# Performance work log

Measured on AMD Instinct MI355X. Metric: run time of the kernel, lower is better.

## Reference

```python
import jax, jax.numpy as jnp
import numpy as np

N = 2_000_000  # total nodes across batch
F = 16         # eigenvector coefficient dim
B = 8          # number of graphs in batch (2^B sign combos)

def setup_inputs() -> dict:
    key = jax.random.key(0)
    k1, k2, k3 = jax.random.split(key, 3)
    inp = jax.random.normal(k1, (N, F), dtype=jnp.float32)
    tgt = jax.random.normal(k2, (N, F), dtype=jnp.float32)
    batch = jnp.sort(jax.random.randint(k3, (N,), 0, B, dtype=jnp.int32))
    return {"input": inp, "target": tgt, "batch": batch, "batch_size": B}

def reference(input, target, batch, batch_size):
    # loss(s) = sum((s_{batch} * x - t)^2) = sum(x^2) + sum(t^2) - 2 * sum_g s_g * dot_g
    # where dot_g = sum_{i in graph g} <x_i, t_i>.  Min over s in {+1,-1}^B is the
    # exact value produced by the original 2^B brute-force loop (reduction='sum').
    per_node = jnp.sum(input * target, axis=-1)                      # [N]
    dots = jax.ops.segment_sum(per_node, batch, num_segments=batch_size)  # [B]
    base = jnp.sum(input * input) + jnp.sum(target * target)         # scalar
    # enumerate all 2^B sign combinations (tiny, graph-level)
    idx = jnp.arange(2 ** batch_size)
    bits = (idx[:, None] >> jnp.arange(batch_size)[None, :]) & 1     # [2^B, B]
    signs = (1 - 2 * bits).astype(dots.dtype)                        # {+1,-1}
    losses = base - 2.0 * (signs @ dots)                             # [2^B]
    return jnp.min(losses)
```

## Files before the change

### kernel.cpp

```cpp
#include <hip/hip_runtime.h>

#define BLOCK 256
#define GRID  2048
#define NGRAPH 8


__global__ __launch_bounds__(BLOCK) void reduce_kernel(
    const float4* __restrict__ x4,
    const float4* __restrict__ t4,
    const int*    __restrict__ batch,
    float* __restrict__ g_acc,
    long long M )
{
    __shared__ float s_dots[NGRAPH];
    __shared__ float s_base;
    const int tid = threadIdx.x;
    if (tid < NGRAPH) s_dots[tid] = 0.0f;
    if (tid == 0)     s_base = 0.0f;
    __syncthreads();

    const long long stride = (long long)gridDim.x * (long long)blockDim.x;
    const long long start  = (long long)blockIdx.x * blockDim.x + tid;
    const long long M_pad = ((M + stride - 1) / stride) * stride;

    float base = 0.0f;

    for (long long e = start; e < M_pad; e += stride) {
        const bool valid = (e < M);
        float4 a = make_float4(0.f, 0.f, 0.f, 0.f);
        float4 c = make_float4(0.f, 0.f, 0.f, 0.f);
        int b = 0;
        if (valid) {
            a = x4[e];
            c = t4[e];
            b = batch[e >> 2];
        }
        base += a.x*a.x + a.y*a.y + a.z*a.z + a.w*a.w
              + c.x*c.x + c.y*c.y + c.z*c.z + c.w*c.w;
        float d = a.x*c.x + a.y*c.y + a.z*c.z + a.w*c.w;

        const int b0 = __builtin_amdgcn_readfirstlane(b);
        if (__all(b == b0)) {
            for (int off = 32; off > 0; off >>= 1)
                d += __shfl_xor(d, off, 64);
            if ((tid & 63) == 0)
                atomicAdd(&s_dots[b0], d);
        } else {
            atomicAdd(&s_dots[b], d);
        }
    }

    for (int off = 32; off > 0; off >>= 1)
        base += __shfl_xor(base, off, 64);
    if ((tid & 63) == 0)
        atomicAdd(&s_base, base);
    __syncthreads();

    if (tid < NGRAPH) atomicAdd(&g_acc[tid], s_dots[tid]);
    if (tid == 0)     atomicAdd(&g_acc[NGRAPH], s_base);
}

__global__ void finalize_kernel(const float* __restrict__ g_acc,
                                float* __restrict__ out)
{
    if (threadIdx.x == 0) {
        float s = 0.0f;
        #pragma unroll
        for (int i = 0; i < NGRAPH; ++i) s += fabsf(g_acc[i]);
        out[0] = g_acc[NGRAPH] - 2.0f * s;
    }
}

extern "C" void kernel_launch(void* const* d_in, const int* in_sizes, int n_in,
                              void* d_out, int out_size, void* d_ws, size_t ws_size,
                              hipStream_t stream) {
    const float* inp   = (const float*)d_in[0];
    const float* tgt   = (const float*)d_in[1];
    const int*   batch = (const int*)d_in[2];

    const long long Nrows = (long long)in_sizes[0] / 16;
    const long long M     = Nrows * 4;

    float* g_acc = (float*)d_ws;
    hipMemsetAsync(g_acc, 0, (NGRAPH + 1) * sizeof(float), stream);

    reduce_kernel<<<GRID, BLOCK, 0, stream>>>(
        (const float4*)inp, (const float4*)tgt, batch, g_acc, M);

    finalize_kernel<<<1, 64, 0, stream>>>(g_acc, (float*)d_out);
}
```

Measured before the change: 305.0 us.

## Use per-thread graph accumulators and fuse finalize via last-block counter

Replaces the per-iteration wave-uniform check, shuffle reduction and shared atomics with eight per-thread register accumulators selected by predication, and reduces them once at the end. The finalize kernel is folded into the reduce kernel through a global arrival counter, so the last block computes the output. This removes per-element shuffle and atomic overhead and one kernel launch, at the cost of more registers and some extra predicated adds per element.

Result: slower. 554.5 us (+81.8%).

```diff
diff --git a/kernel.cpp b/kernel.cpp
--- a/kernel.cpp
+++ b/kernel.cpp
@@ -10,64 +10,61 @@
     const float4* __restrict__ t4,
     const int*    __restrict__ batch,
     float* __restrict__ g_acc,
+    float* __restrict__ out,
     long long M )
 {
-    __shared__ float s_dots[NGRAPH];
-    __shared__ float s_base;
+    __shared__ float s_acc[NGRAPH + 1];
     const int tid = threadIdx.x;
-    if (tid < NGRAPH) s_dots[tid] = 0.0f;
-    if (tid == 0)     s_base = 0.0f;
+    if (tid < NGRAPH + 1) s_acc[tid] = 0.0f;
     __syncthreads();
 
-    const long long stride = (long long)gridDim.x * (long long)blockDim.x;
-    const long long start  = (long long)blockIdx.x * blockDim.x + tid;
-    const long long M_pad = ((M + stride - 1) / stride) * stride;
-
+    float acc[NGRAPH];
+    #pragma unroll
+    for (int i = 0; i < NGRAPH; ++i) acc[i] = 0.0f;
     float base = 0.0f;
 
-    for (long long e = start; e < M_pad; e += stride) {
-        const bool valid = (e < M);
-        float4 a = make_float4(0.f, 0.f, 0.f, 0.f);
-        float4 c = make_float4(0.f, 0.f, 0.f, 0.f);
-        int b = 0;
-        if (valid) {
-            a = x4[e];
-            c = t4[e];
-            b = batch[e >> 2];
-        }
+    const long long stride = (long long)gridDim.x * (long long)blockDim.x;
+    for (long long e = (long long)blockIdx.x * blockDim.x + tid; e < M; e += stride) {
+        const float4 a = x4[e];
+        const float4 c = t4[e];
+        const int   b  = batch[e >> 2];
+
         base += a.x*a.x + a.y*a.y + a.z*a.z + a.w*a.w
               + c.x*c.x + c.y*c.y + c.z*c.z + c.w*c.w;
-        float d = a.x*c.x + a.y*c.y + a.z*c.z + a.w*c.w;
+        const float d = a.x*c.x + a.y*c.y + a.z*c.z + a.w*c.w;
 
-        const int b0 = __builtin_amdgcn_readfirstlane(b);
-        if (__all(b == b0)) {
-            for (int off = 32; off > 0; off >>= 1)
-                d += __shfl_xor(d, off, 64);
-            if ((tid & 63) == 0)
-                atomicAdd(&s_dots[b0], d);
-        } else {
-            atomicAdd(&s_dots[b], d);
-        }
+        #pragma unroll
+        for (int i = 0; i < NGRAPH; ++i)
+            acc[i] += (b == i) ? d : 0.0f;
     }
 
-    for (int off = 32; off > 0; off >>= 1)
-        base += __shfl_xor(base, off, 64);
-    if ((tid & 63) == 0)
-        atomicAdd(&s_base, base);
+    #pragma unroll
+    for (int i = 0; i <= NGRAPH; ++i) {
+        float v = (i < NGRAPH) ? acc[i] : base;
+        #pragma unroll
+        for (int off = 32; off > 0; off >>= 1)
+            v += __shfl_xor(v, off, 64);
+        if ((tid & 63) == 0)
+            atomicAdd(&s_acc[i], v);
+    }
     __syncthreads();
 
-    if (tid < NGRAPH) atomicAdd(&g_acc[tid], s_dots[tid]);
-    if (tid == 0)     atomicAdd(&g_acc[NGRAPH], s_base);
-}
+    if (tid <= NGRAPH)
+        atomicAdd(&g_acc[tid], s_acc[tid]);
 
-__global__ void finalize_kernel(const float* __restrict__ g_acc,
-                                float* __restrict__ out)
-{
-    if (threadIdx.x == 0) {
-        float s = 0.0f;
-        #pragma unroll
-        for (int i = 0; i < NGRAPH; ++i) s += fabsf(g_acc[i]);
-        out[0] = g_acc[NGRAPH] - 2.0f * s;
+    __threadfence();
+    __syncthreads();
+    if (tid == 0) {
+        unsigned* cnt = (unsigned*)&g_acc[NGRAPH + 1];
+        const unsigned old = atomicAdd(cnt, 1u);
+        if (old == (unsigned)gridDim.x - 1u) {
+            float s = 0.0f;
+            #pragma unroll
+            for (int i = 0; i < NGRAPH; ++i)
+                s += fabsf(atomicAdd(&g_acc[i], 0.0f));
+            const float b0 = atomicAdd(&g_acc[NGRAPH], 0.0f);
+            out[0] = b0 - 2.0f * s;
+        }
     }
 }
 
@@ -82,10 +79,9 @@
     const long long M     = Nrows * 4;
 
     float* g_acc = (float*)d_ws;
-    hipMemsetAsync(g_acc, 0, (NGRAPH + 1) * sizeof(float), stream);
+    hipMemsetAsync(g_acc, 0, (NGRAPH + 2) * sizeof(float), stream);
 
     reduce_kernel<<<GRID, BLOCK, 0, stream>>>(
-        (const float4*)inp, (const float4*)tgt, batch, g_acc, M);
-
-    finalize_kernel<<<1, 64, 0, stream>>>(g_acc, (float*)d_out);
+        (const float4*)inp, (const float4*)tgt, batch, g_acc,
+        (float*)d_out, M);
 }
```
